# Kernel optimization log

Measured on AMD Instinct MI355X. Metric: run time of the kernel, lower is better.

Reference implementation:

```python
import jax, jax.numpy as jnp
import numpy as np

B, BS, WS = 2, 1024, 512
D_IN, H, DH, DFF = 2048, 16, 128, 8192
DM = H * DH


def _ln(x, g, eps=1e-5):
    m = x.mean(-1, keepdims=True)
    v = ((x - m) ** 2).mean(-1, keepdims=True)
    return (x - m) / jnp.sqrt(v + eps) * g


def _rotate_half(x):
    p = x.reshape(x.shape[:-1] + (-1, 2))
    a, b = p[..., 0], p[..., 1]
    return jnp.stack([-b, a], axis=-1).reshape(x.shape)


def _rope(x, freqs, scale):
    # xpos convention: align rotary table from the end for shorter sequences
    f = freqs[-x.shape[1]:]
    s = scale[-x.shape[1]:]
    return x * jnp.cos(f) * s + _rotate_half(x) * jnp.sin(f) * s


def setup_inputs():
    key = jax.random.key(0)
    ks = jax.random.split(key, 12)
    def w(k, shape, s=0.02):
        return jax.random.normal(k, shape, dtype=jnp.float32) * s
    x = jax.random.normal(ks[0], (B, BS, D_IN), dtype=jnp.float32)
    cache_k = jnp.zeros((B, WS, DM), jnp.float32)  # first call: zero KV cache
    cache_v = jnp.zeros((B, WS, DM), jnp.float32)
    # rotary frequencies over concatenated length, interleaved pairs
    pos = jnp.arange(BS + WS, dtype=jnp.float32)
    inv = 1.0 / (10000.0 ** (jnp.arange(0, DM, 2, dtype=jnp.float32) / DM))
    rotary = jnp.repeat(pos[:, None] * inv[None, :], 2, axis=-1)  # [BS+WS, DM]
    xscale = jax.random.uniform(ks[1], (BS + WS, DM), jnp.float32, 0.8, 1.2)
    # sliding window mask: query i (abs pos WS+i) sees keys j with i < j <= i+WS
    i = np.arange(BS)[:, None]
    j = np.arange(BS + WS)[None, :]
    mask = jnp.asarray(((j > i) & (j <= i + WS)).astype(np.int32))
    return dict(
        x=x, cache_k=cache_k, cache_v=cache_v, rotary=rotary, xscale=xscale, mask=mask,
        g_in=jnp.ones((D_IN,), jnp.float32),
        Wq=w(ks[2], (DM, D_IN)), Wk=w(ks[3], (DM, D_IN)), Wv=w(ks[4], (DM, D_IN)),
        g_q=jnp.ones((DM,), jnp.float32), g_k=jnp.ones((DM,), jnp.float32),
        Wlq=w(ks[5], (DM, DM)), blq=jnp.zeros((DM,), jnp.float32),
        Wlk=w(ks[6], (DM, DM)), blk=jnp.zeros((DM,), jnp.float32),
        Wlv=w(ks[7], (DM, DM)), blv=jnp.zeros((DM,), jnp.float32),
        Wo=w(ks[8], (DM, DM)), bo=jnp.zeros((DM,), jnp.float32),
        g_ffn=jnp.ones((DM,), jnp.float32),
        W1=w(ks[9], (DFF, DM)), W2=w(ks[10], (D_IN, DFF)))


def reference(x, cache_k, cache_v, rotary, xscale, mask, g_in, Wq, Wk, Wv, g_q, g_k,
              Wlq, blq, Wlk, blk, Wlv, blv, Wo, bo, g_ffn, W1, W2):
    xn = _ln(x, g_in)
    q = _ln(xn @ Wq.T, g_q)            # [B, BS, DM]
    k = _ln(xn @ Wk.T, g_k)
    v = xn @ Wv.T
    k = jnp.concatenate([cache_k, k], axis=1)  # [B, WS+BS, DM]
    v = jnp.concatenate([cache_v, v], axis=1)
    q_r = _rope(q, rotary, xscale)
    k_r = _rope(k, rotary, 1.0 / xscale)
    def heads(t):
        return t.reshape(t.shape[0], -1, H, DH).transpose(0, 2, 1, 3)
    qh = heads(q_r @ Wlq.T + blq)      # [B, H, BS, DH]
    kh = heads(k_r @ Wlk.T + blk)      # [B, H, WS+BS, DH]
    vh = heads(v @ Wlv.T + blv)
    scores = jnp.einsum('bhqd,bhkd->bhqk', qh, kh) / jnp.float32(np.sqrt(DH))
    scores = jnp.where(mask == 0, jnp.float32(-1e9), scores)
    p = jax.nn.softmax(scores, axis=-1)
    o = jnp.einsum('bhqk,bhkd->bhqd', p, vh)
    o = o.transpose(0, 2, 1, 3).reshape(x.shape[0], -1, DM) @ Wo.T + bo
    return jax.nn.relu(_ln(o, g_ffn) @ W1.T) @ W2.T
```

## Files before the change

### kernel.cpp

```cpp
#include <hip/hip_runtime.h>

typedef unsigned short u16;
typedef __attribute__((ext_vector_type(8))) __bf16 bf16x8;
typedef __attribute__((ext_vector_type(4))) float f32x4;

__device__ __forceinline__ float b2f(u16 u) {
    unsigned int i = ((unsigned int)u) << 16;
    return __builtin_bit_cast(float, i);
}
__device__ __forceinline__ u16 f2b(float f) {
    unsigned int x = __builtin_bit_cast(unsigned int, f);
    x += 0x7fffu + ((x >> 16) & 1u);
    return (u16)(x >> 16);
}
__device__ __forceinline__ void gld_lds16(const void* g, void* l) {
    __builtin_amdgcn_global_load_lds(
        (const __attribute__((address_space(1))) unsigned int*)g,
        (__attribute__((address_space(3))) unsigned int*)l, 16, 0, 0);
}

struct CVT3 { const float* s0; u16* d0; const float* s1; u16* d1;
              const float* s2; u16* d2; };
__global__ __launch_bounds__(256) void cvt3_f32_bf16(CVT3 c, int n4)
{
    const float* s = (blockIdx.z == 0) ? c.s0 : ((blockIdx.z == 1) ? c.s1 : c.s2);
    u16* d = (blockIdx.z == 0) ? c.d0 : ((blockIdx.z == 1) ? c.d1 : c.d2);
    int i = blockIdx.x * 256 + threadIdx.x;
    if (i < n4) {
        float4 v = ((const float4*)s)[i];
        ushort4 o;
        o.x = f2b(v.x); o.y = f2b(v.y); o.z = f2b(v.z); o.w = f2b(v.w);
        ((ushort4*)d)[i] = o;
    }
}

__global__ __launch_bounds__(256) void reduce3_into(
    const float* __restrict__ p0, const float* __restrict__ p1,
    const float* __restrict__ p2, float* __restrict__ io, int n4)
{
    int i = blockIdx.x * 256 + threadIdx.x;
    if (i < n4) {
        float4 a = ((const float4*)p0)[i];
        float4 b = ((const float4*)p1)[i];
        float4 c = ((const float4*)p2)[i];
        float4 d = ((float4*)io)[i];
        d.x += a.x + b.x + c.x; d.y += a.y + b.y + c.y;
        d.z += a.z + b.z + c.z; d.w += a.w + b.w + c.w;
        ((float4*)io)[i] = d;
    }
}

enum { EP_BF16 = 0, EP_BF16_BIAS, EP_BF16_RELU, EP_BF16_KV, EP_BF16_BIAS_VT, EP_F32_OUT };

template <int MODE>
__global__ __launch_bounds__(256) void gemm_bt(
    const u16* __restrict__ A, const u16* __restrict__ W,
    const float* __restrict__ bias, void* __restrict__ out,
    int M, int N, int K)
{
    __shared__ u16 As[128 * 64];
    __shared__ u16 Bs[128 * 64];
    const int tid = threadIdx.x;
    const int row0 = blockIdx.y * 128, col0 = blockIdx.x * 128;
    const int wave = tid >> 6, lane = tid & 63, quad = lane >> 4, l16 = lane & 15;
    const int wm = (wave >> 1) * 64, wn = (wave & 1) * 64;

    f32x4 acc[4][4];
#pragma unroll
    for (int i = 0; i < 4; ++i)
#pragma unroll
        for (int j = 0; j < 4; ++j) acc[i][j] = (f32x4){0.f, 0.f, 0.f, 0.f};

    const char* Ab = (const char*)A + (size_t)row0 * K * 2;
    const char* Wb = (const char*)W + (size_t)col0 * K * 2;
    const size_t ldb = (size_t)K * 2;

    for (int k0 = 0; k0 < K; k0 += 64) {
#pragma unroll
        for (int r = 0; r < 4; ++r) {
            int o = r * 4096 + tid * 16;
            int trow = o >> 7, tcolb = o & 127;
            gld_lds16(Ab + (size_t)trow * ldb + (size_t)k0 * 2 + tcolb, (char*)As + o);
            gld_lds16(Wb + (size_t)trow * ldb + (size_t)k0 * 2 + tcolb, (char*)Bs + o);
        }
        __syncthreads();
#pragma unroll
        for (int ks = 0; ks < 2; ++ks) {
            bf16x8 af[4], bfr[4];
#pragma unroll
            for (int i = 0; i < 4; ++i)
                af[i] = *(const bf16x8*)(As + (wm + i * 16 + l16) * 64 + ks * 32 + quad * 8);
#pragma unroll
            for (int j = 0; j < 4; ++j)
                bfr[j] = *(const bf16x8*)(Bs + (wn + j * 16 + l16) * 64 + ks * 32 + quad * 8);
#pragma unroll
            for (int i = 0; i < 4; ++i)
#pragma unroll
                for (int j = 0; j < 4; ++j)
                    acc[i][j] = __builtin_amdgcn_mfma_f32_16x16x32_bf16(af[i], bfr[j], acc[i][j], 0, 0, 0);
        }
        __syncthreads();
    }

#pragma unroll
    for (int j = 0; j < 4; ++j) {
        int gcol = col0 + wn + j * 16 + l16;
        float bv = 0.f;
        if (MODE == EP_BF16_BIAS || MODE == EP_BF16_BIAS_VT) bv = bias[gcol];
#pragma unroll
        for (int i = 0; i < 4; ++i) {
            int growb = row0 + wm + i * 16 + quad * 4;
#pragma unroll
            for (int reg = 0; reg < 4; ++reg) {
                int grow = growb + reg;
                float v = acc[i][j][reg] + bv;
                if (MODE == EP_BF16_RELU) v = fmaxf(v, 0.f);
                if (MODE == EP_F32_OUT) {
                    ((float*)out)[(size_t)grow * N + gcol] = v;
                } else if (MODE == EP_BF16_KV) {
                    int b = grow >> 10, s = grow & 1023;
                    ((u16*)out)[((size_t)(b * 1536 + 512 + s)) * N + gcol] = f2b(v);
                } else if (MODE == EP_BF16_BIAS_VT) {
                    int b = (grow >= 1536) ? 1 : 0;
                    int jk = grow - b * 1536;
                    ((u16*)out)[((size_t)(b * 2048 + gcol)) * 1536 + jk] = f2b(v);
                } else {
                    ((u16*)out)[(size_t)grow * N + gcol] = f2b(v);
                }
            }
        }
    }
}

struct FuseA { const u16* A; const u16* W; const float* bias; void* out; int M; int mode; };
struct Fuse3 { FuseA z0, z1, z2; };

__global__ __launch_bounds__(256) void gemm_bt_f(Fuse3 f, int K)
{
    FuseA p = (blockIdx.z == 0) ? f.z0 : ((blockIdx.z == 1) ? f.z1 : f.z2);
    const int row0 = blockIdx.y * 128, col0 = blockIdx.x * 128;
    if (row0 >= p.M) return;

    __shared__ u16 As[128 * 64];
    __shared__ u16 Bs[128 * 64];
    const int tid = threadIdx.x;
    const int wave = tid >> 6, lane = tid & 63, quad = lane >> 4, l16 = lane & 15;
    const int wm = (wave >> 1) * 64, wn = (wave & 1) * 64;

    f32x4 acc[4][4];
#pragma unroll
    for (int i = 0; i < 4; ++i)
#pragma unroll
        for (int j = 0; j < 4; ++j) acc[i][j] = (f32x4){0.f, 0.f, 0.f, 0.f};

    const char* Ab = (const char*)p.A + (size_t)row0 * K * 2;
    const char* Wb = (const char*)p.W + (size_t)col0 * K * 2;
    const size_t ldb = (size_t)K * 2;

    for (int k0 = 0; k0 < K; k0 += 64) {
#pragma unroll
        for (int r = 0; r < 4; ++r) {
            int o = r * 4096 + tid * 16;
            int trow = o >> 7, tcolb = o & 127;
            gld_lds16(Ab + (size_t)trow * ldb + (size_t)k0 * 2 + tcolb, (char*)As + o);
            gld_lds16(Wb + (size_t)trow * ldb + (size_t)k0 * 2 + tcolb, (char*)Bs + o);
        }
        __syncthreads();
#pragma unroll
        for (int ks = 0; ks < 2; ++ks) {
            bf16x8 af[4], bfr[4];
#pragma unroll
            for (int i = 0; i < 4; ++i)
                af[i] = *(const bf16x8*)(As + (wm + i * 16 + l16) * 64 + ks * 32 + quad * 8);
#pragma unroll
            for (int j = 0; j < 4; ++j)
                bfr[j] = *(const bf16x8*)(Bs + (wn + j * 16 + l16) * 64 + ks * 32 + quad * 8);
#pragma unroll
            for (int i = 0; i < 4; ++i)
#pragma unroll
                for (int j = 0; j < 4; ++j)
                    acc[i][j] = __builtin_amdgcn_mfma_f32_16x16x32_bf16(af[i], bfr[j], acc[i][j], 0, 0, 0);
        }
        __syncthreads();
    }

#pragma unroll
    for (int j = 0; j < 4; ++j) {
        int gcol = col0 + wn + j * 16 + l16;
        float bv = (p.mode == EP_BF16_BIAS || p.mode == EP_BF16_BIAS_VT) ? p.bias[gcol] : 0.f;
#pragma unroll
        for (int i = 0; i < 4; ++i) {
            int growb = row0 + wm + i * 16 + quad * 4;
#pragma unroll
            for (int reg = 0; reg < 4; ++reg) {
                int grow = growb + reg;
                u16 hv = f2b(acc[i][j][reg] + bv);
                size_t idx;
                if (p.mode == EP_BF16_KV) {
                    int b = grow >> 10, s = grow & 1023;
                    idx = ((size_t)(b * 1536 + 512 + s)) * 2048 + gcol;
                } else if (p.mode == EP_BF16_BIAS_VT) {
                    int b = (grow >= 1536) ? 1 : 0;
                    int jk = grow - b * 1536;
                    idx = ((size_t)(b * 2048 + gcol)) * 1536 + jk;
                } else {
                    idx = (size_t)grow * 2048 + gcol;
                }
                ((u16*)p.out)[idx] = hv;
            }
        }
    }
}

struct SKP { const u16* A; const u16* W; const float* bias;
             float* o0; float* o1; float* o2; float* o3; int N, K, Kc; };

__global__ __launch_bounds__(256) void gemm_bt_p(SKP s)
{
    __shared__ u16 As[128 * 64];
    __shared__ u16 Bs[128 * 64];
    const int tid = threadIdx.x;
    const int row0 = blockIdx.y * 128, col0 = blockIdx.x * 128;
    const int wave = tid >> 6, lane = tid & 63, quad = lane >> 4, l16 = lane & 15;
    const int wm = (wave >> 1) * 64, wn = (wave & 1) * 64;
    const int z = blockIdx.z;
    float* out = (z == 0) ? s.o0 : ((z == 1) ? s.o1 : ((z == 2) ? s.o2 : s.o3));
    const int kbeg = z * s.Kc, kend = kbeg + s.Kc;

    f32x4 acc[4][4];
#pragma unroll
    for (int i = 0; i < 4; ++i)
#pragma unroll
        for (int j = 0; j < 4; ++j) acc[i][j] = (f32x4){0.f, 0.f, 0.f, 0.f};

    const char* Ab = (const char*)s.A + (size_t)row0 * s.K * 2;
    const char* Wb = (const char*)s.W + (size_t)col0 * s.K * 2;
    const size_t ldb = (size_t)s.K * 2;

    for (int k0 = kbeg; k0 < kend; k0 += 64) {
#pragma unroll
        for (int r = 0; r < 4; ++r) {
            int o = r * 4096 + tid * 16;
            int trow = o >> 7, tcolb = o & 127;
            gld_lds16(Ab + (size_t)trow * ldb + (size_t)k0 * 2 + tcolb, (char*)As + o);
            gld_lds16(Wb + (size_t)trow * ldb + (size_t)k0 * 2 + tcolb, (char*)Bs + o);
        }
        __syncthreads();
#pragma unroll
        for (int ks = 0; ks < 2; ++ks) {
            bf16x8 af[4], bfr[4];
#pragma unroll
            for (int i = 0; i < 4; ++i)
                af[i] = *(const bf16x8*)(As + (wm + i * 16 + l16) * 64 + ks * 32 + quad * 8);
#pragma unroll
            for (int j = 0; j < 4; ++j)
                bfr[j] = *(const bf16x8*)(Bs + (wn + j * 16 + l16) * 64 + ks * 32 + quad * 8);
#pragma unroll
            for (int i = 0; i < 4; ++i)
#pragma unroll
                for (int j = 0; j < 4; ++j)
                    acc[i][j] = __builtin_amdgcn_mfma_f32_16x16x32_bf16(af[i], bfr[j], acc[i][j], 0, 0, 0);
        }
        __syncthreads();
    }

#pragma unroll
    for (int j = 0; j < 4; ++j) {
        int gcol = col0 + wn + j * 16 + l16;
        float bv = (s.bias != nullptr && z == 0) ? s.bias[gcol] : 0.f;
#pragma unroll
        for (int i = 0; i < 4; ++i) {
            int growb = row0 + wm + i * 16 + quad * 4;
#pragma unroll
            for (int reg = 0; reg < 4; ++reg) {
                int grow = growb + reg;
                out[(size_t)grow * s.N + gcol] = acc[i][j][reg] + bv;
            }
        }
    }
}

template <int IN_F32>
__global__ __launch_bounds__(256) void ln_rows(
    const void* __restrict__ in, const float* __restrict__ gamma,
    u16* __restrict__ out)
{
    const int row = blockIdx.x, tid = threadIdx.x;
    const float* inf = (const float*)in + (size_t)row * 2048;
    const u16* inb = (const u16*)in + (size_t)row * 2048;
    float v[8], s1 = 0.f, s2 = 0.f;
#pragma unroll
    for (int i = 0; i < 8; ++i) {
        int c = tid + i * 256;
        float x = IN_F32 ? inf[c] : b2f(inb[c]);
        v[i] = x; s1 += x; s2 += x * x;
    }
#pragma unroll
    for (int off = 32; off >= 1; off >>= 1) { s1 += __shfl_xor(s1, off, 64); s2 += __shfl_xor(s2, off, 64); }
    __shared__ float ra[4], rb[4];
    int wave = tid >> 6, lane = tid & 63;
    if (lane == 0) { ra[wave] = s1; rb[wave] = s2; }
    __syncthreads();
    s1 = ra[0] + ra[1] + ra[2] + ra[3];
    s2 = rb[0] + rb[1] + rb[2] + rb[3];
    float mean = s1 * (1.f / 2048.f);
    float var = s2 * (1.f / 2048.f) - mean * mean;
    float rstd = rsqrtf(var + 1e-5f);
#pragma unroll
    for (int i = 0; i < 8; ++i) {
        int c = tid + i * 256;
        out[(size_t)row * 2048 + c] = f2b((v[i] - mean) * rstd * gamma[c]);
    }
}

__global__ __launch_bounds__(256) void ln4_rows(
    const float* __restrict__ p0, const float* __restrict__ p1,
    const float* __restrict__ p2, const float* __restrict__ p3,
    const float* __restrict__ gamma, u16* __restrict__ out)
{
    const int row = blockIdx.x, tid = threadIdx.x;
    const size_t rb_ = (size_t)row * 2048;
    float v[8], s1 = 0.f, s2 = 0.f;
#pragma unroll
    for (int i = 0; i < 8; ++i) {
        int c = tid + i * 256;
        float x = p0[rb_ + c] + p1[rb_ + c] + p2[rb_ + c] + p3[rb_ + c];
        v[i] = x; s1 += x; s2 += x * x;
    }
#pragma unroll
    for (int off = 32; off >= 1; off >>= 1) { s1 += __shfl_xor(s1, off, 64); s2 += __shfl_xor(s2, off, 64); }
    __shared__ float ra[4], rbs[4];
    int wave = tid >> 6, lane = tid & 63;
    if (lane == 0) { ra[wave] = s1; rbs[wave] = s2; }
    __syncthreads();
    s1 = ra[0] + ra[1] + ra[2] + ra[3];
    s2 = rbs[0] + rbs[1] + rbs[2] + rbs[3];
    float mean = s1 * (1.f / 2048.f);
    float rstd = rsqrtf(s2 * (1.f / 2048.f) - mean * mean + 1e-5f);
#pragma unroll
    for (int i = 0; i < 8; ++i) {
        int c = tid + i * 256;
        out[rb_ + c] = f2b((v[i] - mean) * rstd * gamma[c]);
    }
}

__global__ __launch_bounds__(256) void qk_post(
    const u16* __restrict__ qpre, const u16* __restrict__ kpre,
    const float* __restrict__ gq, const float* __restrict__ gk,
    const float* __restrict__ rotary, const float* __restrict__ xscale,
    u16* __restrict__ qrope, u16* __restrict__ kfull)
{
    const int is_k = blockIdx.x & 1;
    const int row = blockIdx.x >> 1;
    const int b = row >> 10, s = row & 1023;
    const int tid = threadIdx.x, base = tid * 8;
    const u16* in = (is_k ? kpre : qpre) + (size_t)row * 2048;
    float v[8], s1 = 0.f, s2 = 0.f;
#pragma unroll
    for (int i = 0; i < 8; ++i) { float x = b2f(in[base + i]); v[i] = x; s1 += x; s2 += x * x; }
#pragma unroll
    for (int off = 32; off >= 1; off >>= 1) { s1 += __shfl_xor(s1, off, 64); s2 += __shfl_xor(s2, off, 64); }
    __shared__ float ra[4], rb[4];
    int wave = tid >> 6, lane = tid & 63;
    if (lane == 0) { ra[wave] = s1; rb[wave] = s2; }
    __syncthreads();
    s1 = ra[0] + ra[1] + ra[2] + ra[3];
    s2 = rb[0] + rb[1] + rb[2] + rb[3];
    float mean = s1 * (1.f / 2048.f);
    float rstd = rsqrtf(s2 * (1.f / 2048.f) - mean * mean + 1e-5f);
    const float* g = is_k ? gk : gq;
    const int rr = 512 + s;
    u16* outp = is_k ? (kfull + ((size_t)(b * 1536 + 512 + s)) * 2048)
                     : (qrope + (size_t)row * 2048);
#pragma unroll
    for (int p = 0; p < 4; ++p) {
        int e0 = base + 2 * p, e1 = e0 + 1;
        float x0 = (v[2 * p] - mean) * rstd * g[e0];
        float x1 = (v[2 * p + 1] - mean) * rstd * g[e1];
        float f = rotary[(size_t)rr * 2048 + e0];
        float sn, cs; sincosf(f, &sn, &cs);
        float sc0 = xscale[(size_t)rr * 2048 + e0];
        float sc1 = xscale[(size_t)rr * 2048 + e1];
        if (is_k) { sc0 = 1.f / sc0; sc1 = 1.f / sc1; }
        outp[e0] = f2b((x0 * cs - x1 * sn) * sc0);
        outp[e1] = f2b((x1 * cs + x0 * sn) * sc1);
    }
}

__global__ __launch_bounds__(256) void cache_prep(
    const float* __restrict__ cache_k, const float* __restrict__ cache_v,
    const float* __restrict__ rotary, const float* __restrict__ xscale,
    u16* __restrict__ kfull, u16* __restrict__ vfull)
{
    const int row = blockIdx.x;
    const int b = row >> 9, j = row & 511;
    const int base = threadIdx.x * 8;
    const float* ck = cache_k + ((size_t)row) * 2048;
    const float* cv = cache_v + ((size_t)row) * 2048;
    u16* ko = kfull + ((size_t)(b * 1536 + j)) * 2048;
    u16* vo = vfull + ((size_t)(b * 1536 + j)) * 2048;
#pragma unroll
    for (int p = 0; p < 4; ++p) {
        int e0 = base + 2 * p, e1 = e0 + 1;
        float x0 = ck[e0], x1 = ck[e1];
        float f = rotary[(size_t)j * 2048 + e0];
        float sn, cs; sincosf(f, &sn, &cs);
        float sc0 = 1.f / xscale[(size_t)j * 2048 + e0];
        float sc1 = 1.f / xscale[(size_t)j * 2048 + e1];
        ko[e0] = f2b((x0 * cs - x1 * sn) * sc0);
        ko[e1] = f2b((x1 * cs + x0 * sn) * sc1);
        vo[e0] = f2b(cv[e0]); vo[e1] = f2b(cv[e1]);
    }
}

__global__ __launch_bounds__(256) void attn(
    const u16* __restrict__ qh, const u16* __restrict__ kh,
    const u16* __restrict__ vt, u16* __restrict__ o)
{
    __shared__ u16 Qs[16 * 128];
    __shared__ float Ss[16 * 544];
    __shared__ u16 Ps[16 * 544];
    __shared__ float Ls[16];
    const int qt = blockIdx.x, h = blockIdx.y, b = blockIdx.z;
    const int i0 = qt * 16;
    const int tid = threadIdx.x;
    const int wave = tid >> 6, lane = tid & 63, quad = lane >> 4, l16 = lane & 15;

    {
        int r = tid >> 4, seg = tid & 15;
        const u16* src = qh + ((size_t)(b * 1024 + i0 + r)) * 2048 + h * 128 + seg * 8;
        *(uint4*)(Qs + r * 128 + seg * 8) = *(const uint4*)src;
    }
    __syncthreads();

    const float sm = 0.08838834764831845f;
    for (int kt = wave; kt < 33; kt += 4) {
        int jb = i0 + kt * 16;
        const u16* krow = kh + ((size_t)(b * 1536 + jb + l16)) * 2048 + h * 128 + quad * 8;
        const u16* qrow = Qs + l16 * 128 + quad * 8;
        f32x4 sacc = (f32x4){0.f, 0.f, 0.f, 0.f};
#pragma unroll
        for (int st = 0; st < 4; ++st) {
            bf16x8 aq = *(const bf16x8*)(qrow + st * 32);
            bf16x8 bk = *(const bf16x8*)(krow + st * 32);
            sacc = __builtin_amdgcn_mfma_f32_16x16x32_bf16(aq, bk, sacc, 0, 0, 0);
        }
        int jj = jb + l16;
#pragma unroll
        for (int reg = 0; reg < 4; ++reg) {
            int qi = i0 + quad * 4 + reg;
            bool valid = (jj > qi) && (jj <= qi + 512);
            Ss[(quad * 4 + reg) * 544 + kt * 16 + l16] = valid ? sacc[reg] * sm : -1e9f;
        }
    }
    __syncthreads();

    {
        int g = tid >> 4, l = tid & 15;
        float m = -1e30f;
        for (int j = l; j < 528; j += 16) m = fmaxf(m, Ss[g * 544 + j]);
#pragma unroll
        for (int off = 8; off >= 1; off >>= 1) m = fmaxf(m, __shfl_xor(m, off, 16));
        float sum = 0.f;
        for (int j = l; j < 528; j += 16) {
            float e = __expf(Ss[g * 544 + j] - m);
            sum += e;
            Ps[g * 544 + j] = f2b(e);
        }
        Ps[g * 544 + 528 + l] = 0;
#pragma unroll
        for (int off = 8; off >= 1; off >>= 1) sum += __shfl_xor(sum, off, 16);
        if (l == 0) Ls[g] = sum;
    }
    __syncthreads();

    f32x4 oa0 = (f32x4){0.f, 0.f, 0.f, 0.f}, oa1 = oa0;
    const u16* vbase = vt + ((size_t)(b * 2048 + h * 128 + wave * 32 + l16)) * 1536 + i0;
    for (int jc = 0; jc < 17; ++jc) {
        bf16x8 pf = *(const bf16x8*)(Ps + l16 * 544 + jc * 32 + quad * 8);
        bf16x8 v0 = *(const bf16x8*)(vbase + jc * 32 + quad * 8);
        bf16x8 v1 = *(const bf16x8*)(vbase + (size_t)16 * 1536 + jc * 32 + quad * 8);
        oa0 = __builtin_amdgcn_mfma_f32_16x16x32_bf16(pf, v0, oa0, 0, 0, 0);
        oa1 = __builtin_amdgcn_mfma_f32_16x16x32_bf16(pf, v1, oa1, 0, 0, 0);
    }
#pragma unroll
    for (int reg = 0; reg < 4; ++reg) {
        int q = quad * 4 + reg;
        float inv = 1.f / Ls[q];
        size_t orow = ((size_t)(b * 1024 + i0 + q)) * 2048 + h * 128 + wave * 32;
        o[orow + l16] = f2b(oa0[reg] * inv);
        o[orow + 16 + l16] = f2b(oa1[reg] * inv);
    }
}

extern "C" void kernel_launch(void* const* d_in, const int* in_sizes, int n_in,
                              void* d_out, int out_size, void* d_ws, size_t ws_size,
                              hipStream_t stream)
{
    const float* x       = (const float*)d_in[0];
    const float* cache_k = (const float*)d_in[1];
    const float* cache_v = (const float*)d_in[2];
    const float* rotary  = (const float*)d_in[3];
    const float* xscale  = (const float*)d_in[4];
    const float* g_in = (const float*)d_in[6];
    const float* Wq   = (const float*)d_in[7];
    const float* Wk   = (const float*)d_in[8];
    const float* Wv   = (const float*)d_in[9];
    const float* g_q  = (const float*)d_in[10];
    const float* g_k  = (const float*)d_in[11];
    const float* Wlq  = (const float*)d_in[12];
    const float* blq  = (const float*)d_in[13];
    const float* Wlk  = (const float*)d_in[14];
    const float* blk  = (const float*)d_in[15];
    const float* Wlv  = (const float*)d_in[16];
    const float* blv  = (const float*)d_in[17];
    const float* Wo   = (const float*)d_in[18];
    const float* bo   = (const float*)d_in[19];
    const float* g_ffn= (const float*)d_in[20];
    const float* W1   = (const float*)d_in[21];
    const float* W2   = (const float*)d_in[22];

    char* ws = (char*)d_ws;
    u16* xn     = (u16*)(ws + 0);
    u16* qpre   = (u16*)(ws + 8388608);
    u16* kpre   = (u16*)(ws + 16777216);
    u16* wq_b   = (u16*)(ws + 25165824);
    u16* khb    = (u16*)(ws + 25165824);
    u16* vfull  = (u16*)(ws + 37748736);
    u16* wv_b   = (u16*)(ws + 50331648);
    u16* kfull  = (u16*)(ws + 50331648);
    u16* wk_b   = (u16*)(ws + 62914560);
    u16* vt     = (u16*)(ws + 62914560);
    u16* qrope  = (u16*)(ws + 75563008);
    u16* wlq_b  = (u16*)(ws + 83951616);
    u16* wlk_b  = (u16*)(ws + 92340224);
    u16* wlv_b  = (u16*)(ws + 100728832);
    u16* h2     = (u16*)(ws + 83951616);
    u16* qhb    = qpre;
    u16* obuf   = xn;
    u16* h1     = qrope;
    u16* wo_b   = (u16*)(ws + 25165824);
    u16* w1_b   = (u16*)(ws + 0);
    u16* w2_b   = (u16*)(ws + 0);
    float* WP0  = (float*)(ws + 33554432);
    float* WP1  = (float*)(ws + 50331648);
    float* WP2  = (float*)(ws + 83951616);
    float* WP3  = (float*)(ws + 8388608);
    float* FP0  = (float*)(ws + 33554432);
    float* FP1  = (float*)(ws + 50331648);
    float* FP2  = (float*)(ws + 67108864);

    const int N1M = 4194304 / 4;
    const int N4M = 16777216 / 4;

    ln_rows<1><<<2048, 256, 0, stream>>>(x, g_in, xn);
    cvt3_f32_bf16<<<dim3(N1M / 256, 1, 3), 256, 0, stream>>>(
        CVT3{Wq, wq_b, Wk, wk_b, Wv, wv_b}, N1M);

    Fuse3 fq;
    fq.z0 = FuseA{xn, wq_b, nullptr, (void*)qpre,  2048, EP_BF16};
    fq.z1 = FuseA{xn, wk_b, nullptr, (void*)kpre,  2048, EP_BF16};
    fq.z2 = FuseA{xn, wv_b, nullptr, (void*)vfull, 2048, EP_BF16_KV};
    gemm_bt_f<<<dim3(16, 16, 3), 256, 0, stream>>>(fq, 2048);

    cache_prep<<<1024, 256, 0, stream>>>(cache_k, cache_v, rotary, xscale, kfull, vfull);
    qk_post<<<4096, 256, 0, stream>>>(qpre, kpre, g_q, g_k, rotary, xscale, qrope, kfull);
    cvt3_f32_bf16<<<dim3(N1M / 256, 1, 3), 256, 0, stream>>>(
        CVT3{Wlq, wlq_b, Wlk, wlk_b, Wlv, wlv_b}, N1M);

    Fuse3 fl;
    fl.z0 = FuseA{qrope, wlq_b, blq, (void*)qhb, 2048, EP_BF16_BIAS};
    fl.z1 = FuseA{kfull, wlk_b, blk, (void*)khb, 3072, EP_BF16_BIAS};
    fl.z2 = FuseA{vfull, wlv_b, blv, (void*)vt,  3072, EP_BF16_BIAS_VT};
    gemm_bt_f<<<dim3(16, 24, 3), 256, 0, stream>>>(fl, 2048);

    attn<<<dim3(64, 16, 2), 256, 0, stream>>>(qhb, khb, vt, obuf);

    cvt3_f32_bf16<<<dim3(N1M / 256, 1, 1), 256, 0, stream>>>(
        CVT3{Wo, wo_b, Wo, wo_b, Wo, wo_b}, N1M);
    gemm_bt_p<<<dim3(16, 16, 4), 256, 0, stream>>>(
        SKP{obuf, wo_b, bo, WP0, WP1, WP2, WP3, 2048, 2048, 512});
    ln4_rows<<<2048, 256, 0, stream>>>(WP0, WP1, WP2, WP3, g_ffn, h1);

    cvt3_f32_bf16<<<dim3(N4M / 256, 1, 1), 256, 0, stream>>>(
        CVT3{W1, w1_b, W1, w1_b, W1, w1_b}, N4M);
    gemm_bt<EP_BF16_RELU><<<dim3(64, 16), 256, 0, stream>>>(h1, w1_b, nullptr, h2, 2048, 8192, 2048);

    cvt3_f32_bf16<<<dim3(N4M / 256, 1, 1), 256, 0, stream>>>(
        CVT3{W2, w2_b, W2, w2_b, W2, w2_b}, N4M);
    gemm_bt_p<<<dim3(16, 16, 4), 256, 0, stream>>>(
        SKP{h2, w2_b, nullptr, FP0, FP1, FP2, (float*)d_out, 2048, 8192, 2048});
    reduce3_into<<<N1M / 256, 256, 0, stream>>>(FP0, FP1, FP2, (float*)d_out, N1M);
}
```

Baseline: 908.9 us.

## Double-buffer GEMM LDS tiles with XOR swizzle and shared core loop

The three bf16 GEMM kernels now share one main loop. It splits the K tile to 32 and double-buffers the LDS tiles, so async global-to-LDS loads for the next step are issued while MFMAs run on the current buffer. Each iteration now has one barrier instead of two. An XOR swizzle on the 16-byte column chunk is meant to reduce LDS bank conflicts on fragment reads. The trade-off is a shorter K step with more loop overhead and a barrier for every 32 K.

Measured after the change: 880.7 us. 1.03x faster.

```diff
diff --git a/kernel.cpp b/kernel.cpp
--- a/kernel.cpp
+++ b/kernel.cpp
@@ -52,17 +52,68 @@
 
 enum { EP_BF16 = 0, EP_BF16_BIAS, EP_BF16_RELU, EP_BF16_KV, EP_BF16_BIAS_VT, EP_F32_OUT };
 
+__device__ __forceinline__ void gemm_core(
+    const u16* __restrict__ Ab, const u16* __restrict__ Wb,
+    int ldk, int kbeg, int kend, int tid,
+    u16 (&As)[2][4096], u16 (&Bs)[2][4096], f32x4 (&acc)[4][4])
+{
+    const int lane = tid & 63, quad = lane >> 4, l16 = lane & 15;
+    const int wave = tid >> 6;
+    const int wm = (wave >> 1) * 64, wn = (wave & 1) * 64;
+    const int srow = tid >> 2;
+    const int sc = (tid & 3) ^ (srow & 3);
+    const int xorc = (quad ^ (l16 & 3)) * 16;
+
+    const u16* pa0 = Ab + (size_t)srow * ldk + kbeg + sc * 8;
+    const u16* pa1 = pa0 + (size_t)64 * ldk;
+    const u16* pb0 = Wb + (size_t)srow * ldk + kbeg + sc * 8;
+    const u16* pb1 = pb0 + (size_t)64 * ldk;
+    char* dA = (char*)&As[0][0] + tid * 16;
+    char* dB = (char*)&Bs[0][0] + tid * 16;
+
+    gld_lds16(pa0, dA); gld_lds16(pa1, dA + 4096);
+    gld_lds16(pb0, dB); gld_lds16(pb1, dB + 4096);
+    __syncthreads();
+
+    int cur = 0;
+    const int nk = kend - kbeg;
+    for (int ko = 0; ko < nk; ko += 32) {
+        if (ko + 32 < nk) {
+            int kn = ko + 32, nb = cur ^ 1;
+            gld_lds16(pa0 + kn, dA + nb * 8192);
+            gld_lds16(pa1 + kn, dA + nb * 8192 + 4096);
+            gld_lds16(pb0 + kn, dB + nb * 8192);
+            gld_lds16(pb1 + kn, dB + nb * 8192 + 4096);
+        }
+        bf16x8 af[4], bfr[4];
+#pragma unroll
+        for (int i = 0; i < 4; ++i)
+            af[i] = *(const bf16x8*)((const char*)&As[cur][0] + (wm + i * 16 + l16) * 64 + xorc);
+#pragma unroll
+        for (int j = 0; j < 4; ++j)
+            bfr[j] = *(const bf16x8*)((const char*)&Bs[cur][0] + (wn + j * 16 + l16) * 64 + xorc);
+#pragma unroll
+        for (int i = 0; i < 4; ++i)
+#pragma unroll
+            for (int j = 0; j < 4; ++j)
+                acc[i][j] = __builtin_amdgcn_mfma_f32_16x16x32_bf16(af[i], bfr[j], acc[i][j], 0, 0, 0);
+        __syncthreads();
+        cur ^= 1;
+    }
+}
+
 template <int MODE>
 __global__ __launch_bounds__(256) void gemm_bt(
     const u16* __restrict__ A, const u16* __restrict__ W,
     const float* __restrict__ bias, void* __restrict__ out,
     int M, int N, int K)
 {
-    __shared__ u16 As[128 * 64];
-    __shared__ u16 Bs[128 * 64];
+    __shared__ u16 As[2][4096];
+    __shared__ u16 Bs[2][4096];
     const int tid = threadIdx.x;
     const int row0 = blockIdx.y * 128, col0 = blockIdx.x * 128;
-    const int wave = tid >> 6, lane = tid & 63, quad = lane >> 4, l16 = lane & 15;
+    const int lane = tid & 63, quad = lane >> 4, l16 = lane & 15;
+    const int wave = tid >> 6;
     const int wm = (wave >> 1) * 64, wn = (wave & 1) * 64;
 
     f32x4 acc[4][4];
@@ -71,36 +122,7 @@
 #pragma unroll
         for (int j = 0; j < 4; ++j) acc[i][j] = (f32x4){0.f, 0.f, 0.f, 0.f};
 
-    const char* Ab = (const char*)A + (size_t)row0 * K * 2;
-    const char* Wb = (const char*)W + (size_t)col0 * K * 2;
-    const size_t ldb = (size_t)K * 2;
-
-    for (int k0 = 0; k0 < K; k0 += 64) {
-#pragma unroll
-        for (int r = 0; r < 4; ++r) {
-            int o = r * 4096 + tid * 16;
-            int trow = o >> 7, tcolb = o & 127;
-            gld_lds16(Ab + (size_t)trow * ldb + (size_t)k0 * 2 + tcolb, (char*)As + o);
-            gld_lds16(Wb + (size_t)trow * ldb + (size_t)k0 * 2 + tcolb, (char*)Bs + o);
-        }
-        __syncthreads();
-#pragma unroll
-        for (int ks = 0; ks < 2; ++ks) {
-            bf16x8 af[4], bfr[4];
-#pragma unroll
-            for (int i = 0; i < 4; ++i)
-                af[i] = *(const bf16x8*)(As + (wm + i * 16 + l16) * 64 + ks * 32 + quad * 8);
-#pragma unroll
-            for (int j = 0; j < 4; ++j)
-                bfr[j] = *(const bf16x8*)(Bs + (wn + j * 16 + l16) * 64 + ks * 32 + quad * 8);
-#pragma unroll
-            for (int i = 0; i < 4; ++i)
-#pragma unroll
-                for (int j = 0; j < 4; ++j)
-                    acc[i][j] = __builtin_amdgcn_mfma_f32_16x16x32_bf16(af[i], bfr[j], acc[i][j], 0, 0, 0);
-        }
-        __syncthreads();
-    }
+    gemm_core(A + (size_t)row0 * K, W + (size_t)col0 * K, K, 0, K, tid, As, Bs, acc);
 
 #pragma unroll
     for (int j = 0; j < 4; ++j) {
@@ -141,10 +163,11 @@
     const int row0 = blockIdx.y * 128, col0 = blockIdx.x * 128;
     if (row0 >= p.M) return;
 
-    __shared__ u16 As[128 * 64];
-    __shared__ u16 Bs[128 * 64];
+    __shared__ u16 As[2][4096];
+    __shared__ u16 Bs[2][4096];
     const int tid = threadIdx.x;
-    const int wave = tid >> 6, lane = tid & 63, quad = lane >> 4, l16 = lane & 15;
+    const int lane = tid & 63, quad = lane >> 4, l16 = lane & 15;
+    const int wave = tid >> 6;
     const int wm = (wave >> 1) * 64, wn = (wave & 1) * 64;
 
     f32x4 acc[4][4];
@@ -153,36 +176,7 @@
 #pragma unroll
         for (int j = 0; j < 4; ++j) acc[i][j] = (f32x4){0.f, 0.f, 0.f, 0.f};
 
-    const char* Ab = (const char*)p.A + (size_t)row0 * K * 2;
-    const char* Wb = (const char*)p.W + (size_t)col0 * K * 2;
-    const size_t ldb = (size_t)K * 2;
-
-    for (int k0 = 0; k0 < K; k0 += 64) {
-#pragma unroll
-        for (int r = 0; r < 4; ++r) {
-            int o = r * 4096 + tid * 16;
-            int trow = o >> 7, tcolb = o & 127;
-            gld_lds16(Ab + (size_t)trow * ldb + (size_t)k0 * 2 + tcolb, (char*)As + o);
-            gld_lds16(Wb + (size_t)trow * ldb + (size_t)k0 * 2 + tcolb, (char*)Bs + o);
-        }
-        __syncthreads();
-#pragma unroll
-        for (int ks = 0; ks < 2; ++ks) {
-            bf16x8 af[4], bfr[4];
-#pragma unroll
-            for (int i = 0; i < 4; ++i)
-                af[i] = *(const bf16x8*)(As + (wm + i * 16 + l16) * 64 + ks * 32 + quad * 8);
-#pragma unroll
-            for (int j = 0; j < 4; ++j)
-                bfr[j] = *(const bf16x8*)(Bs + (wn + j * 16 + l16) * 64 + ks * 32 + quad * 8);
-#pragma unroll
-            for (int i = 0; i < 4; ++i)
-#pragma unroll
-                for (int j = 0; j < 4; ++j)
-                    acc[i][j] = __builtin_amdgcn_mfma_f32_16x16x32_bf16(af[i], bfr[j], acc[i][j], 0, 0, 0);
-        }
-        __syncthreads();
-    }
+    gemm_core(p.A + (size_t)row0 * K, p.W + (size_t)col0 * K, K, 0, K, tid, As, Bs, acc);
 
 #pragma unroll
     for (int j = 0; j < 4; ++j) {
@@ -217,11 +211,12 @@
 
 __global__ __launch_bounds__(256) void gemm_bt_p(SKP s)
 {
-    __shared__ u16 As[128 * 64];
-    __shared__ u16 Bs[128 * 64];
+    __shared__ u16 As[2][4096];
+    __shared__ u16 Bs[2][4096];
     const int tid = threadIdx.x;
     const int row0 = blockIdx.y * 128, col0 = blockIdx.x * 128;
-    const int wave = tid >> 6, lane = tid & 63, quad = lane >> 4, l16 = lane & 15;
+    const int lane = tid & 63, quad = lane >> 4, l16 = lane & 15;
+    const int wave = tid >> 6;
     const int wm = (wave >> 1) * 64, wn = (wave & 1) * 64;
     const int z = blockIdx.z;
     float* out = (z == 0) ? s.o0 : ((z == 1) ? s.o1 : ((z == 2) ? s.o2 : s.o3));
@@ -233,36 +228,8 @@
 #pragma unroll
         for (int j = 0; j < 4; ++j) acc[i][j] = (f32x4){0.f, 0.f, 0.f, 0.f};
 
-    const char* Ab = (const char*)s.A + (size_t)row0 * s.K * 2;
-    const char* Wb = (const char*)s.W + (size_t)col0 * s.K * 2;
-    const size_t ldb = (size_t)s.K * 2;
-
-    for (int k0 = kbeg; k0 < kend; k0 += 64) {
-#pragma unroll
-        for (int r = 0; r < 4; ++r) {
-            int o = r * 4096 + tid * 16;
-            int trow = o >> 7, tcolb = o & 127;
-            gld_lds16(Ab + (size_t)trow * ldb + (size_t)k0 * 2 + tcolb, (char*)As + o);
-            gld_lds16(Wb + (size_t)trow * ldb + (size_t)k0 * 2 + tcolb, (char*)Bs + o);
-        }
-        __syncthreads();
-#pragma unroll
-        for (int ks = 0; ks < 2; ++ks) {
-            bf16x8 af[4], bfr[4];
-#pragma unroll
-            for (int i = 0; i < 4; ++i)
-                af[i] = *(const bf16x8*)(As + (wm + i * 16 + l16) * 64 + ks * 32 + quad * 8);
-#pragma unroll
-            for (int j = 0; j < 4; ++j)
-                bfr[j] = *(const bf16x8*)(Bs + (wn + j * 16 + l16) * 64 + ks * 32 + quad * 8);
-#pragma unroll
-            for (int i = 0; i < 4; ++i)
-#pragma unroll
-                for (int j = 0; j < 4; ++j)
-                    acc[i][j] = __builtin_amdgcn_mfma_f32_16x16x32_bf16(af[i], bfr[j], acc[i][j], 0, 0, 0);
-        }
-        __syncthreads();
-    }
+    gemm_core(s.A + (size_t)row0 * s.K, s.W + (size_t)col0 * s.K, s.K,
+              kbeg, kend, tid, As, Bs, acc);
 
 #pragma unroll
     for (int j = 0; j < 4; ++j) {
```
